# Performance work log

Measured on AMD Instinct MI355X. Metric: run time of the kernel, lower is better.

Reference implementation:

```python
import jax, jax.numpy as jnp
import numpy as np

T, B, H = 512, 256, 256


def setup_inputs() -> dict:
    key = jax.random.key(0)
    k1, k2, k3, k4 = jax.random.split(key, 4)
    ins = jax.random.normal(k1, (T, B, H), jnp.float32)
    resets = jax.random.randint(k2, (T, B), 0, 2) > 0  # bool reset mask
    carry = jnp.zeros((B, H), jnp.float32)
    scale = 1.0 / np.sqrt(H).astype(np.float32)
    # Fused GRU weights: columns ordered [r | z | n] for input and hidden projections.
    Wi = jax.random.normal(k3, (H, 3 * H), jnp.float32) * scale  # dense_i kernels (ir, iz, in)
    Wh = jax.random.normal(k4, (H, 3 * H), jnp.float32) * scale  # dense_h kernels (hr, hz, hn)
    bi = jnp.zeros((3 * H,), jnp.float32)   # dense_i biases (ir, iz, in)
    bhn = jnp.zeros((H,), jnp.float32)      # dense_h bias, only the 'hn' gate has one in flax GRUCell
    return dict(ins=ins, resets=resets, carry=carry, Wi=Wi, bi=bi, Wh=Wh, bhn=bhn)


def reference(ins, resets, carry, Wi, bi, Wh, bhn):
    """Faithful jax version of ScannedRNN: per-step reset-masked flax GRUCell scan.

    flax GRUCell math:
      r = sigmoid(x@Wir + bir + h@Whr)
      z = sigmoid(x@Wiz + biz + h@Whz)
      n = tanh(x@Win + bin + r * (h@Whn + bhn))
      h' = (1-z)*n + z*h ; output y = h'
    Reset mask zeroes the carry before the cell (initialize_carry -> zeros).
    """
    def step(h, xt):
        x, reset = xt  # x: [B,H], reset: [B]
        h = jnp.where(reset[:, None], jnp.zeros_like(h), h)
        gi = x @ Wi + bi          # [B, 3H]
        gh = h @ Wh               # [B, 3H]
        ir_, iz_, in_ = jnp.split(gi, 3, axis=-1)
        hr_, hz_, hn_ = jnp.split(gh, 3, axis=-1)
        r = jax.nn.sigmoid(ir_ + hr_)
        z = jax.nn.sigmoid(iz_ + hz_)
        n = jnp.tanh(in_ + r * (hn_ + bhn))
        h_new = (1.0 - z) * n + z * h
        return h_new, h_new

    _, ys = jax.lax.scan(step, carry, (ins, resets))
    return ys  # [T, B, H]
```

## Files before the change

### kernel.cpp

```cpp
#include <hip/hip_runtime.h>
#include <stdint.h>


typedef __attribute__((ext_vector_type(8))) __bf16 bf16x8;
typedef __attribute__((ext_vector_type(4))) float f32x4;

__device__ __forceinline__ float bf2f(unsigned short u) {
    union { unsigned int i; float f; } v; v.i = ((unsigned int)u) << 16; return v.f;
}
__device__ __forceinline__ unsigned short f2bf(float f) {
    union { float f; unsigned int i; } v; v.f = f;
    unsigned int x = v.i;
    x = x + 0x7fffu + ((x >> 16) & 1u);
    return (unsigned short)(x >> 16);
}
__device__ __forceinline__ float fsig(float x) {
    return __builtin_amdgcn_rcpf(1.f + __builtin_amdgcn_exp2f(-1.442695041f * x));
}
__device__ __forceinline__ float ftanh(float x) {
    return 1.f - 2.f * __builtin_amdgcn_rcpf(1.f + __builtin_amdgcn_exp2f(2.885390082f * x));
}

__global__ void prep_weights(const float* __restrict__ Wi, const float* __restrict__ Wh,
                             unsigned short* __restrict__ WiT, unsigned short* __restrict__ WhT) {
    const int idx = blockIdx.x * 256 + threadIdx.x;
    const float* src = blockIdx.y ? Wh : Wi;
    unsigned short* dst = blockIdx.y ? WhT : WiT;
    const int c = idx >> 8, k = idx & 255;
    dst[c * 256 + k] = f2bf(src[k * 768 + c]);
}

__device__ __forceinline__ void stage_wn(const unsigned short* __restrict__ WT,
                                         unsigned short* __restrict__ s_wn, int tid) {
#pragma unroll
    for (int w = 0; w < 16; ++w) {
        const int gi = tid + w * 512;
        const int c = gi >> 5, gr = gi & 31;
        bf16x8 v = *(const bf16x8*)(WT + (size_t)(512 + c) * 256 + gr * 8);
        *(bf16x8*)(&s_wn[(c * 32 + (gr ^ (c & 7))) * 8]) = v;
    }
}

__launch_bounds__(512, 2)
__global__ void gi_gemm(const float* __restrict__ ins, const unsigned short* __restrict__ WiT,
                        const float* __restrict__ bi, unsigned int* __restrict__ GI32) {
    __shared__ unsigned short s_wn[65536];

    const int tid = threadIdx.x;
    const int lane = tid & 63, wv = tid >> 6;
    const int quad = lane >> 4, n16 = lane & 15;

    stage_wn(WiT, s_wn, tid);

    bf16x8 wfrag[2][2][8];
#pragma unroll
    for (int g = 0; g < 2; ++g)
#pragma unroll
        for (int tl = 0; tl < 2; ++tl) {
            const int c = g * 256 + wv * 32 + tl * 16 + n16;
            const unsigned short* src = WiT + c * 256 + quad * 8;
#pragma unroll
            for (int kt = 0; kt < 8; ++kt)
                wfrag[g][tl][kt] = *(const bf16x8*)(src + kt * 32);
        }
    float bi_r[3][2];
#pragma unroll
    for (int g = 0; g < 3; ++g)
#pragma unroll
        for (int tl = 0; tl < 2; ++tl)
            bi_r[g][tl] = bi[g * 256 + wv * 32 + tl * 16 + n16];

    const int key = n16 & 7;
    const int c0row = (wv * 32 + n16) * 32;
    const int c1row = (wv * 32 + 16 + n16) * 32;

    __syncthreads();

    for (int i = 0; i < 32; ++i) {
        const int chunk = blockIdx.x + i * 256;
        const float* arow = ins + ((size_t)chunk * 16 + n16) * 256 + quad * 8;
        bf16x8 af[8];
#pragma unroll
        for (int kt = 0; kt < 8; ++kt) {
            const float4 q0 = *(const float4*)(arow + kt * 32);
            const float4 q1 = *(const float4*)(arow + kt * 32 + 4);
            bf16x8 v;
            v[0] = (__bf16)q0.x; v[1] = (__bf16)q0.y; v[2] = (__bf16)q0.z; v[3] = (__bf16)q0.w;
            v[4] = (__bf16)q1.x; v[5] = (__bf16)q1.y; v[6] = (__bf16)q1.z; v[7] = (__bf16)q1.w;
            af[kt] = v;
        }

        f32x4 acc[3][2] = {};
#pragma unroll
        for (int kt = 0; kt < 8; ++kt) {
#pragma unroll
            for (int g = 0; g < 2; ++g)
#pragma unroll
                for (int tl = 0; tl < 2; ++tl)
                    acc[g][tl] = __builtin_amdgcn_mfma_f32_16x16x32_bf16(af[kt], wfrag[g][tl][kt], acc[g][tl], 0, 0, 0);
            const int gsw = ((kt * 4 + quad) ^ key) * 8;
            const bf16x8 bn0 = *(const bf16x8*)(&s_wn[(c0row * 8) + gsw]);
            const bf16x8 bn1 = *(const bf16x8*)(&s_wn[(c1row * 8) + gsw]);
            acc[2][0] = __builtin_amdgcn_mfma_f32_16x16x32_bf16(af[kt], bn0, acc[2][0], 0, 0, 0);
            acc[2][1] = __builtin_amdgcn_mfma_f32_16x16x32_bf16(af[kt], bn1, acc[2][1], 0, 0, 0);
        }

        {
            const int t = chunk >> 4;
            const int b0 = (chunk & 15) * 16;
#pragma unroll
            for (int g = 0; g < 3; ++g)
#pragma unroll
                for (int r = 0; r < 4; ++r) {
                    const unsigned int lo = f2bf(acc[g][0][r] + bi_r[g][0]);
                    const unsigned int hi = f2bf(acc[g][1][r] + bi_r[g][1]);
                    GI32[((size_t)t * 256 + b0 + quad * 4 + r) * 384 + g * 128 + wv * 16 + n16] =
                        lo | (hi << 16);
                }
        }
    }
}

__launch_bounds__(512, 2)
__global__ void gru_scan(const unsigned short* __restrict__ GI, const int* __restrict__ resets,
                         const float* __restrict__ carry, const unsigned short* __restrict__ WhT,
                         const float* __restrict__ bhn, float* __restrict__ out) {
    __shared__ int s_reset[512];
    __shared__ unsigned short s_h[2][16 * 264];
    __shared__ unsigned short s_wn[65536];

    const int b = blockIdx.x;
    const int tid = threadIdx.x;
    const int lane = tid & 63, wv = tid >> 6;
    const int quad = lane >> 4, n16 = lane & 15;

    s_reset[tid] = resets[tid * 256 + b];
    stage_wn(WhT, s_wn, tid);

    bf16x8 wfrag[2][2][8];
#pragma unroll
    for (int g = 0; g < 2; ++g)
#pragma unroll
        for (int tl = 0; tl < 2; ++tl) {
            const int c = g * 256 + wv * 32 + tl * 16 + n16;
            const unsigned short* src = WhT + c * 256 + quad * 8;
#pragma unroll
            for (int kt = 0; kt < 8; ++kt)
                wfrag[g][tl][kt] = *(const bf16x8*)(src + kt * 32);
        }
    float bhn_r[2];
    bhn_r[0] = bhn[wv * 32 + n16];
    bhn_r[1] = bhn[wv * 32 + 16 + n16];

    const int key = n16 & 7;
    const int c0row = (wv * 32 + n16) * 32;
    const int c1row = (wv * 32 + 16 + n16) * 32;

    __syncthreads();

    int t_cur[4], t_end[4];
    float h_prev[2][4];
#pragma unroll
    for (int r = 0; r < 4; ++r) {
        const int slot = quad * 4 + r;
        const int w0 = slot * 32;
        int st = -1;
        for (int t = w0; t < w0 + 32; ++t)
            if (t == 0 || s_reset[t] != 0) { st = t; break; }
        int en = 511;
        for (int t = w0 + 32; t < 512; ++t)
            if (s_reset[t] != 0) { en = t - 1; break; }
        float h0 = 0.f, h1 = 0.f;
        if (st == 0 && s_reset[0] == 0) {
            h0 = carry[b * 256 + wv * 32 + n16];
            h1 = carry[b * 256 + wv * 32 + 16 + n16];
        }
        if (st < 0) { t_cur[r] = 1; t_end[r] = 0; }
        else        { t_cur[r] = st; t_end[r] = en; }
        h_prev[0][r] = h0; h_prev[1][r] = h1;
        s_h[0][slot * 264 + wv * 32 + n16] = f2bf(h0);
        s_h[0][slot * 264 + wv * 32 + 16 + n16] = f2bf(h1);
    }

    const unsigned int* GI32b = (const unsigned int*)GI + (size_t)b * 384 + (wv * 16 + n16);
    unsigned int gva[4][3], gvb[4][3];
#pragma unroll
    for (int r = 0; r < 4; ++r) {
        const int tr0 = (t_cur[r] <= t_end[r]) ? t_cur[r] : 0;
        const unsigned int* gp = GI32b + (size_t)tr0 * 98304;
        gva[r][0] = gp[0]; gva[r][1] = gp[128]; gva[r][2] = gp[256];
    }

    __syncthreads();

#define SCAN_STEP(GCUR, GNXT)                                                                   \
    {                                                                                           \
        const bool any_ = (t_cur[0] <= t_end[0]) | (t_cur[1] <= t_end[1]) |                     \
                          (t_cur[2] <= t_end[2]) | (t_cur[3] <= t_end[3]);                      \
        if (__ballot((int)any_) == 0ull) break;                                                 \
                                     \
        _Pragma("unroll")                                                                       \
        for (int r = 0; r < 4; ++r) {                                                           \
            const int trn = (t_cur[r] < t_end[r]) ? (t_cur[r] + 1) : 0;                         \
            const unsigned int* gp = GI32b + (size_t)trn * 98304;                               \
            GNXT[r][0] = gp[0]; GNXT[r][1] = gp[128]; GNXT[r][2] = gp[256];                     \
        }                                                                                       \
                                                           \
        f32x4 acc2[3][2] = {};                                                                  \
        _Pragma("unroll")                                                                       \
        for (int kt = 0; kt < 8; ++kt) {                                                        \
            bf16x8 af = *(const bf16x8*)(&s_h[buf][n16 * 264 + kt * 32 + quad * 8]);            \
            _Pragma("unroll")                                                                   \
            for (int g = 0; g < 2; ++g)                                                         \
                _Pragma("unroll")                                                               \
                for (int tl = 0; tl < 2; ++tl)                                                  \
                    acc2[g][tl] = __builtin_amdgcn_mfma_f32_16x16x32_bf16(af, wfrag[g][tl][kt], acc2[g][tl], 0, 0, 0); \
            const int gsw = ((kt * 4 + quad) ^ key) * 8;                                        \
            const bf16x8 bn0 = *(const bf16x8*)(&s_wn[(c0row * 8) + gsw]);                      \
            const bf16x8 bn1 = *(const bf16x8*)(&s_wn[(c1row * 8) + gsw]);                      \
            acc2[2][0] = __builtin_amdgcn_mfma_f32_16x16x32_bf16(af, bn0, acc2[2][0], 0, 0, 0); \
            acc2[2][1] = __builtin_amdgcn_mfma_f32_16x16x32_bf16(af, bn1, acc2[2][1], 0, 0, 0); \
        }                                                                                       \
                                                              \
        float hn[2][4];                                                                         \
        _Pragma("unroll")                                                                       \
        for (int r = 0; r < 4; ++r) {                                                           \
            const bool alive = t_cur[r] <= t_end[r];                                            \
            const unsigned int ur = GCUR[r][0], uz = GCUR[r][1], un = GCUR[r][2];               \
            _Pragma("unroll")                                                                   \
            for (int tl = 0; tl < 2; ++tl) {                                                    \
                const int c = wv * 32 + tl * 16 + n16;                                          \
                const float gr = bf2f((unsigned short)(tl ? (ur >> 16) : (ur & 0xffffu)));      \
                const float gz = bf2f((unsigned short)(tl ? (uz >> 16) : (uz & 0xffffu)));      \
                const float gn = bf2f((unsigned short)(tl ? (un >> 16) : (un & 0xffffu)));      \
                const float rr = fsig(gr + acc2[0][tl][r]);                                     \
                const float zz = fsig(gz + acc2[1][tl][r]);                                     \
                const float nn = ftanh(gn + rr * (acc2[2][tl][r] + bhn_r[tl]));                 \
                hn[tl][r] = (1.f - zz) * nn + zz * h_prev[tl][r];                               \
                if (alive) out[((size_t)t_cur[r] * 256 + b) * 256 + c] = hn[tl][r];             \
            }                                                                                   \
        }                                                                                       \
                                                   \
        _Pragma("unroll")                                                                       \
        for (int r = 0; r < 4; ++r) {                                                           \
            const int slot = quad * 4 + r;                                                      \
            const bool alive = t_cur[r] <= t_end[r];                                            \
            const int tn = t_cur[r] + 1;                                                        \
            const bool nalive = alive && (tn <= t_end[r]);                                      \
            float k0 = 0.f, k1 = 0.f;                                                           \
            if (nalive && s_reset[tn & 511] == 0) { k0 = hn[0][r]; k1 = hn[1][r]; }             \
            h_prev[0][r] = k0; h_prev[1][r] = k1;                                               \
            s_h[buf ^ 1][slot * 264 + wv * 32 + n16] = f2bf(k0);                                \
            s_h[buf ^ 1][slot * 264 + wv * 32 + 16 + n16] = f2bf(k1);                           \
            if (alive) t_cur[r] = tn;                                                           \
        }                                                                                       \
        __syncthreads();                           \
        buf ^= 1;                                                                               \
    }

    int buf = 0;
    for (int it2 = 0; it2 < 260; ++it2) {
        SCAN_STEP(gva, gvb)
        SCAN_STEP(gvb, gva)
    }
#undef SCAN_STEP
}

extern "C" void kernel_launch(void* const* d_in, const int* in_sizes, int n_in,
                              void* d_out, int out_size, void* d_ws, size_t ws_size,
                              hipStream_t stream) {
    const float* ins   = (const float*)d_in[0];
    const int* resets  = (const int*)d_in[1];
    const float* carry = (const float*)d_in[2];
    const float* Wi    = (const float*)d_in[3];
    const float* bi    = (const float*)d_in[4];
    const float* Wh    = (const float*)d_in[5];
    const float* bhn   = (const float*)d_in[6];
    float* out = (float*)d_out;

    unsigned short* WiT = (unsigned short*)d_ws;
    unsigned short* WhT = WiT + 196608;
    unsigned short* GI  = WhT + 196608;

    prep_weights<<<dim3(768, 2), dim3(256), 0, stream>>>(Wi, Wh, WiT, WhT);
    gi_gemm<<<dim3(256), dim3(512), 0, stream>>>(ins, WiT, bi, (unsigned int*)GI);
    gru_scan<<<dim3(256), dim3(512), 0, stream>>>(GI, resets, carry, WhT, bhn, out);
}
```

Before: 494.2 us.

## Keep all three gate weight slices in registers and stage GEMM inputs via LDS

Both kernels now hold the full [r|z|n] weight fragments in registers, so the LDS-staged swizzled n-gate weights and their per-step LDS reads are gone. Launch bounds drop to one block per CU so the larger register footprint fits. The input GEMM instead converts each 16-row activation tile to bf16 into a double-buffered LDS tile, prefetching the next tile into registers. Plain __syncthreads is replaced with an inline-asm lgkmcnt wait plus barrier. The trade is lower occupancy and higher register pressure, with a risk of spills, in exchange for less LDS traffic on the serial scan's critical path.

Result: slower. 532.4 us (+7.7%).

```diff
diff --git a/kernel.cpp b/kernel.cpp
--- a/kernel.cpp
+++ b/kernel.cpp
@@ -4,6 +4,8 @@
 
 typedef __attribute__((ext_vector_type(8))) __bf16 bf16x8;
 typedef __attribute__((ext_vector_type(4))) float f32x4;
+
+#define BAR_LGKM() asm volatile("s_waitcnt lgkmcnt(0)\n\ts_barrier" ::: "memory")
 
 __device__ __forceinline__ float bf2f(unsigned short u) {
     union { unsigned int i; float f; } v; v.i = ((unsigned int)u) << 16; return v.f;
@@ -30,31 +32,18 @@
     dst[c * 256 + k] = f2bf(src[k * 768 + c]);
 }
 
-__device__ __forceinline__ void stage_wn(const unsigned short* __restrict__ WT,
-                                         unsigned short* __restrict__ s_wn, int tid) {
-#pragma unroll
-    for (int w = 0; w < 16; ++w) {
-        const int gi = tid + w * 512;
-        const int c = gi >> 5, gr = gi & 31;
-        bf16x8 v = *(const bf16x8*)(WT + (size_t)(512 + c) * 256 + gr * 8);
-        *(bf16x8*)(&s_wn[(c * 32 + (gr ^ (c & 7))) * 8]) = v;
-    }
-}
-
-__launch_bounds__(512, 2)
+__launch_bounds__(512, 1)
 __global__ void gi_gemm(const float* __restrict__ ins, const unsigned short* __restrict__ WiT,
                         const float* __restrict__ bi, unsigned int* __restrict__ GI32) {
-    __shared__ unsigned short s_wn[65536];
+    __shared__ unsigned short a_buf[2][16 * 264];
 
     const int tid = threadIdx.x;
     const int lane = tid & 63, wv = tid >> 6;
     const int quad = lane >> 4, n16 = lane & 15;
 
-    stage_wn(WiT, s_wn, tid);
-
-    bf16x8 wfrag[2][2][8];
-#pragma unroll
-    for (int g = 0; g < 2; ++g)
+    bf16x8 wfrag[3][2][8];
+#pragma unroll
+    for (int g = 0; g < 3; ++g)
 #pragma unroll
         for (int tl = 0; tl < 2; ++tl) {
             const int c = g * 256 + wv * 32 + tl * 16 + n16;
@@ -70,41 +59,40 @@
         for (int tl = 0; tl < 2; ++tl)
             bi_r[g][tl] = bi[g * 256 + wv * 32 + tl * 16 + n16];
 
-    const int key = n16 & 7;
-    const int c0row = (wv * 32 + n16) * 32;
-    const int c1row = (wv * 32 + 16 + n16) * 32;
-
-    __syncthreads();
-
+    const int srow = tid >> 5;
+    const int scol = (tid & 31) * 8;
+
+    float4 p0, p1;
+    {
+        const float* p = ins + (size_t)blockIdx.x * 16 * 256 + tid * 8;
+        p0 = *(const float4*)p; p1 = *(const float4*)(p + 4);
+    }
+
+    int buf = 0;
     for (int i = 0; i < 32; ++i) {
         const int chunk = blockIdx.x + i * 256;
-        const float* arow = ins + ((size_t)chunk * 16 + n16) * 256 + quad * 8;
-        bf16x8 af[8];
+        {
+            bf16x8 av;
+            av[0] = (__bf16)p0.x; av[1] = (__bf16)p0.y; av[2] = (__bf16)p0.z; av[3] = (__bf16)p0.w;
+            av[4] = (__bf16)p1.x; av[5] = (__bf16)p1.y; av[6] = (__bf16)p1.z; av[7] = (__bf16)p1.w;
+            *(bf16x8*)(&a_buf[buf][srow * 264 + scol]) = av;
+        }
+        if (i + 1 < 32) {
+            const float* p = ins + (size_t)(blockIdx.x + (i + 1) * 256) * 16 * 256 + tid * 8;
+            p0 = *(const float4*)p; p1 = *(const float4*)(p + 4);
+        }
+        BAR_LGKM();
+
+        f32x4 acc[3][2] = {};
 #pragma unroll
         for (int kt = 0; kt < 8; ++kt) {
-            const float4 q0 = *(const float4*)(arow + kt * 32);
-            const float4 q1 = *(const float4*)(arow + kt * 32 + 4);
-            bf16x8 v;
-            v[0] = (__bf16)q0.x; v[1] = (__bf16)q0.y; v[2] = (__bf16)q0.z; v[3] = (__bf16)q0.w;
-            v[4] = (__bf16)q1.x; v[5] = (__bf16)q1.y; v[6] = (__bf16)q1.z; v[7] = (__bf16)q1.w;
-            af[kt] = v;
-        }
-
-        f32x4 acc[3][2] = {};
-#pragma unroll
-        for (int kt = 0; kt < 8; ++kt) {
-#pragma unroll
-            for (int g = 0; g < 2; ++g)
+            bf16x8 af = *(const bf16x8*)(&a_buf[buf][n16 * 264 + kt * 32 + quad * 8]);
+#pragma unroll
+            for (int g = 0; g < 3; ++g)
 #pragma unroll
                 for (int tl = 0; tl < 2; ++tl)
-                    acc[g][tl] = __builtin_amdgcn_mfma_f32_16x16x32_bf16(af[kt], wfrag[g][tl][kt], acc[g][tl], 0, 0, 0);
-            const int gsw = ((kt * 4 + quad) ^ key) * 8;
-            const bf16x8 bn0 = *(const bf16x8*)(&s_wn[(c0row * 8) + gsw]);
-            const bf16x8 bn1 = *(const bf16x8*)(&s_wn[(c1row * 8) + gsw]);
-            acc[2][0] = __builtin_amdgcn_mfma_f32_16x16x32_bf16(af[kt], bn0, acc[2][0], 0, 0, 0);
-            acc[2][1] = __builtin_amdgcn_mfma_f32_16x16x32_bf16(af[kt], bn1, acc[2][1], 0, 0, 0);
-        }
-
+                    acc[g][tl] = __builtin_amdgcn_mfma_f32_16x16x32_bf16(af, wfrag[g][tl][kt], acc[g][tl], 0, 0, 0);
+        }
         {
             const int t = chunk >> 4;
             const int b0 = (chunk & 15) * 16;
@@ -118,16 +106,16 @@
                         lo | (hi << 16);
                 }
         }
-    }
-}
-
-__launch_bounds__(512, 2)
+        buf ^= 1;
+    }
+}
+
+__launch_bounds__(512, 1)
 __global__ void gru_scan(const unsigned short* __restrict__ GI, const int* __restrict__ resets,
                          const float* __restrict__ carry, const unsigned short* __restrict__ WhT,
                          const float* __restrict__ bhn, float* __restrict__ out) {
     __shared__ int s_reset[512];
     __shared__ unsigned short s_h[2][16 * 264];
-    __shared__ unsigned short s_wn[65536];
 
     const int b = blockIdx.x;
     const int tid = threadIdx.x;
@@ -135,11 +123,10 @@
     const int quad = lane >> 4, n16 = lane & 15;
 
     s_reset[tid] = resets[tid * 256 + b];
-    stage_wn(WhT, s_wn, tid);
-
-    bf16x8 wfrag[2][2][8];
-#pragma unroll
-    for (int g = 0; g < 2; ++g)
+
+    bf16x8 wfrag[3][2][8];
+#pragma unroll
+    for (int g = 0; g < 3; ++g)
 #pragma unroll
         for (int tl = 0; tl < 2; ++tl) {
             const int c = g * 256 + wv * 32 + tl * 16 + n16;
@@ -152,11 +139,7 @@
     bhn_r[0] = bhn[wv * 32 + n16];
     bhn_r[1] = bhn[wv * 32 + 16 + n16];
 
-    const int key = n16 & 7;
-    const int c0row = (wv * 32 + n16) * 32;
-    const int c1row = (wv * 32 + 16 + n16) * 32;
-
-    __syncthreads();
+    BAR_LGKM();
 
     int t_cur[4], t_end[4];
     float h_prev[2][4];
@@ -191,14 +174,15 @@
         gva[r][0] = gp[0]; gva[r][1] = gp[128]; gva[r][2] = gp[256];
     }
 
-    __syncthreads();
+    BAR_LGKM();
 
 #define SCAN_STEP(GCUR, GNXT)                                                                   \
     {                                                                                           \
         const bool any_ = (t_cur[0] <= t_end[0]) | (t_cur[1] <= t_end[1]) |                     \
                           (t_cur[2] <= t_end[2]) | (t_cur[3] <= t_end[3]);                      \
         if (__ballot((int)any_) == 0ull) break;                                                 \
-                                     \
+                      \
+                      \
         _Pragma("unroll")                                                                       \
         for (int r = 0; r < 4; ++r) {                                                           \
             const int trn = (t_cur[r] < t_end[r]) ? (t_cur[r] + 1) : 0;                         \
@@ -211,17 +195,12 @@
         for (int kt = 0; kt < 8; ++kt) {                                                        \
             bf16x8 af = *(const bf16x8*)(&s_h[buf][n16 * 264 + kt * 32 + quad * 8]);            \
             _Pragma("unroll")                                                                   \
-            for (int g = 0; g < 2; ++g)                                                         \
+            for (int g = 0; g < 3; ++g)                                                         \
                 _Pragma("unroll")                                                               \
                 for (int tl = 0; tl < 2; ++tl)                                                  \
                     acc2[g][tl] = __builtin_amdgcn_mfma_f32_16x16x32_bf16(af, wfrag[g][tl][kt], acc2[g][tl], 0, 0, 0); \
-            const int gsw = ((kt * 4 + quad) ^ key) * 8;                                        \
-            const bf16x8 bn0 = *(const bf16x8*)(&s_wn[(c0row * 8) + gsw]);                      \
-            const bf16x8 bn1 = *(const bf16x8*)(&s_wn[(c1row * 8) + gsw]);                      \
-            acc2[2][0] = __builtin_amdgcn_mfma_f32_16x16x32_bf16(af, bn0, acc2[2][0], 0, 0, 0); \
-            acc2[2][1] = __builtin_amdgcn_mfma_f32_16x16x32_bf16(af, bn1, acc2[2][1], 0, 0, 0); \
-        }                                                                                       \
-                                                              \
+        }                                                                                       \
+                            \
         float hn[2][4];                                                                         \
         _Pragma("unroll")                                                                       \
         for (int r = 0; r < 4; ++r) {                                                           \
@@ -254,7 +233,7 @@
             s_h[buf ^ 1][slot * 264 + wv * 32 + 16 + n16] = f2bf(k1);                           \
             if (alive) t_cur[r] = tn;                                                           \
         }                                                                                       \
-        __syncthreads();                           \
+        BAR_LGKM();                            \
         buf ^= 1;                                                                               \
     }
 
```
